# Performance work log

Hardware: AMD Instinct MI355X
Metric: run time of the kernel (lower is better)

## Reference

```python
import math
import jax, jax.numpy as jnp
import numpy as np

B, LA, LB, H = 32, 1024, 1024, 1024


def setup_inputs() -> dict:
    key = jax.random.key(0)
    k1, k2, k3, k4 = jax.random.split(key, 4)
    a = jax.random.normal(k1, (B, LA, H), dtype=jnp.float32)
    b = jax.random.normal(k2, (B, LB, H), dtype=jnp.float32)
    mask_a = jax.random.randint(k3, (B, LA, 1), 0, 2, dtype=jnp.int32)
    mask_b = jax.random.randint(k4, (B, LB, 1), 0, 2, dtype=jnp.int32)
    temperature = jnp.asarray(1.0 / math.sqrt(H), dtype=jnp.float32)
    return {"a": a, "b": b, "mask_a": mask_a, "mask_b": mask_b,
            "temperature": temperature}


def reference(a, b, mask_a, mask_b, temperature):
    # attn: [B, La, Lb] scaled cross-attention scores
    attn = jnp.einsum("bsh,bth->bst", a, b) * temperature
    # outer product of per-token validity -> pairwise valid mask [B, La, Lb]
    mask = jnp.einsum("bsi,bti->bst",
                      mask_a.astype(jnp.float32),
                      mask_b.astype(jnp.float32)).astype(bool)
    attn = jnp.where(mask, attn, jnp.float32(-10000.0))
    attn_a = jax.nn.softmax(attn, axis=1)  # normalize over La
    attn_b = jax.nn.softmax(attn, axis=2)  # normalize over Lb
    feature_b = jnp.einsum("bst,bsh->bth", attn_a, a)  # [B, Lb, H]
    feature_a = jnp.einsum("bst,bth->bsh", attn_b, b)  # [B, La, H]
    return feature_a, feature_b
```

## Files before the change

### kernel.cpp

```cpp
#include <hip/hip_runtime.h>

#define NB 32
#define L 1024
#define H 1024

typedef __attribute__((ext_vector_type(4))) float floatx4;
typedef __attribute__((ext_vector_type(8))) short shortx8;
typedef __attribute__((ext_vector_type(8))) unsigned short ushortx8;

__device__ __forceinline__ unsigned short f2bf(float f) {
    union { float f; unsigned int u; } v; v.f = f;
    unsigned int u = v.u;
    u += 0x7fffu + ((u >> 16) & 1u);
    return (unsigned short)(u >> 16);
}
__device__ __forceinline__ float bf2f(unsigned short h) {
    union { unsigned int u; float f; } v; v.u = ((unsigned int)h) << 16;
    return v.f;
}

__device__ __forceinline__ void gload_lds16(const void* g, void* l) {
    __builtin_amdgcn_global_load_lds(
        (const __attribute__((address_space(1))) unsigned int*)g,
        (__attribute__((address_space(3))) unsigned int*)l, 16, 0, 0);
}

__device__ __forceinline__ void swz_tile(int nb, int& bi_l, int& tx, int& ty) {
    int fid = blockIdx.x;
    int wid = (fid & 7) * (nb * 8) + (fid >> 3);
    bi_l = wid >> 6;
    int t = wid & 63;
    tx = t & 7;
    ty = t >> 3;
}

__global__ void detect_kernel(const unsigned short* a, int* flag) {
    int tid = threadIdx.x;
    unsigned short u = a[tid];
    int e = (u >> 7) & 0xff;
    int ok = (u == 0) || (e >= 116 && e <= 136);
    unsigned long long ball = __ballot(ok != 0);
    if (tid == 0) flag[0] = (__popcll(ball) >= 56) ? 1 : 0;
}

__device__ __forceinline__ void store_out(void* out, size_t eidx, float v, int isbf) {
    if (isbf) ((unsigned short*)out)[eidx] = f2bf(v);
    else      ((float*)out)[eidx] = v;
}

__global__ __launch_bounds__(256) void convT_kernel(
    const void* A, const void* Bm, const int* flag,
    unsigned short* a_c, unsigned short* b_c,
    unsigned short* aT, unsigned short* bT,
    float* mean_a, float* mean_b, int b0) {
    __shared__ __align__(16) unsigned short T[64][80];
    int z = blockIdx.z;
    int which = z & 1, bi_l = z >> 1, bi = b0 + bi_l;
    int s0 = blockIdx.y * 64, h0 = blockIdx.x * 64;
    const void* src = which ? Bm : A;
    unsigned short* xc = which ? b_c : a_c;
    unsigned short* xT = which ? bT : aT;
    float* msum = which ? mean_b : mean_a;
    int isbf = flag[0];
    int tid = threadIdx.x;

    int r = tid >> 2, c0 = (tid & 3) * 16;
    size_t gin = (size_t)bi * L * H + (size_t)(s0 + r) * H + h0 + c0;
    unsigned short v[16];
    if (isbf) {
        const unsigned short* p = (const unsigned short*)src + gin;
        *(ushortx8*)&v[0] = *(const ushortx8*)p;
        *(ushortx8*)&v[8] = *(const ushortx8*)(p + 8);
    } else {
        const float* p = (const float*)src + gin;
#pragma unroll
        for (int u = 0; u < 16; u += 4) {
            float4 f = *(const float4*)(p + u);
            v[u] = f2bf(f.x); v[u + 1] = f2bf(f.y);
            v[u + 2] = f2bf(f.z); v[u + 3] = f2bf(f.w);
        }
    }
    *(ushortx8*)&T[r][c0] = *(const ushortx8*)&v[0];
    *(ushortx8*)&T[r][c0 + 8] = *(const ushortx8*)&v[8];
    if (!isbf) {
        size_t gco = (size_t)bi_l * L * H + (size_t)(s0 + r) * H + h0 + c0;
        *(ushortx8*)&xc[gco] = *(const ushortx8*)&v[0];
        *(ushortx8*)&xc[gco + 8] = *(const ushortx8*)&v[8];
    }
    __syncthreads();

    int hr = tid >> 2, sc0 = (tid & 3) * 16;
    unsigned short tv2[16];
    float ms = 0.f;
#pragma unroll
    for (int u = 0; u < 16; ++u) {
        unsigned short q = T[sc0 + u][hr];
        tv2[u] = q;
        ms += bf2f(q);
    }
    size_t gto = (size_t)bi_l * (size_t)H * L + (size_t)(h0 + hr) * L + s0 + sc0;
    *(ushortx8*)&xT[gto] = *(const ushortx8*)&tv2[0];
    *(ushortx8*)&xT[gto + 8] = *(const ushortx8*)&tv2[8];
    ms += __shfl_xor(ms, 1);
    ms += __shfl_xor(ms, 2);
    if ((tid & 3) == 0) atomicAdd(&msum[bi * H + h0 + hr], ms);
}

__device__ __forceinline__ void gemm_kk(
    const unsigned short* Arow, const unsigned short* Brow,
    int lda, int ldb, int K,
    unsigned short* AsBase, unsigned short* BsBase,
    int tid, floatx4 (&acc)[4][4]) {
    int lane = tid & 63;
    int wid = tid >> 6;
    int wm = wid >> 1, wn = wid & 1;
    int lane15 = lane & 15, quad = lane >> 4;

    for (int k0 = 0; k0 < K; k0 += 32) {
#pragma unroll
        for (int it = 0; it < 4; ++it) {
            int idx = (it & 1) * 256 + tid;
            int rr = idx >> 2, cc = (idx & 3) * 8;
            const unsigned short* src = (it < 2)
                ? (Arow + (size_t)rr * lda + k0 + cc)
                : (Brow + (size_t)rr * ldb + k0 + cc);
            unsigned short* dst = ((it < 2) ? AsBase : BsBase) + idx * 8;
            gload_lds16(src, dst);
        }
        __syncthreads();
        shortx8 af[4], bfr[4];
#pragma unroll
        for (int i = 0; i < 4; ++i)
            af[i] = *(const shortx8*)(AsBase + (wm * 64 + i * 16 + lane15) * 32 + quad * 8);
#pragma unroll
        for (int j = 0; j < 4; ++j)
            bfr[j] = *(const shortx8*)(BsBase + (wn * 64 + j * 16 + lane15) * 32 + quad * 8);
#pragma unroll
        for (int i = 0; i < 4; ++i)
#pragma unroll
            for (int j = 0; j < 4; ++j)
                acc[i][j] = __builtin_amdgcn_mfma_f32_16x16x32_bf16(af[i], bfr[j], acc[i][j], 0, 0, 0);
        __syncthreads();
    }
}

__global__ __launch_bounds__(256) void score_kernel(
    const void* Araw, const void* Braw,
    const unsigned short* a_c, const unsigned short* b_c,
    const int* mask_a, const int* mask_b, const void* temp, const int* flag,
    unsigned short* w, unsigned short* wT,
    float* row_l, float* col_l, int b0, int nb) {
    __shared__ __align__(16) unsigned short lds_all[8192];
    unsigned short* As = lds_all;
    unsigned short* Bs = lds_all + 4096;
    int bi_l, tx, ty;
    swz_tile(nb, bi_l, tx, ty);
    int bi = b0 + bi_l;
    int s0 = ty * 128, t0 = tx * 128;
    int tid = threadIdx.x;
    int isbf = flag[0];

    floatx4 acc[4][4];
#pragma unroll
    for (int i = 0; i < 4; ++i)
#pragma unroll
        for (int j = 0; j < 4; ++j)
#pragma unroll
            for (int rr = 0; rr < 4; ++rr) acc[i][j][rr] = 0.f;

    const unsigned short* Arow = isbf
        ? (const unsigned short*)Araw + (size_t)bi * L * H + (size_t)s0 * H
        : a_c + (size_t)bi_l * L * H + (size_t)s0 * H;
    const unsigned short* Brow = isbf
        ? (const unsigned short*)Braw + (size_t)bi * L * H + (size_t)t0 * H
        : b_c + (size_t)bi_l * L * H + (size_t)t0 * H;
    gemm_kk(Arow, Brow, H, H, H, As, Bs, tid, acc);

    float tv = isbf ? bf2f(((const unsigned short*)temp)[0]) : ((const float*)temp)[0];
    int lane = tid & 63, wid = tid >> 6;
    int wm = wid >> 1, wn = wid & 1;
    int lane15 = lane & 15, quad = lane >> 4;

    int mb[4];
#pragma unroll
    for (int j = 0; j < 4; ++j)
        mb[j] = mask_b[bi * L + t0 + wn * 64 + j * 16 + lane15];
    size_t wbase = (size_t)bi_l * L * L;
    float colp[4] = {0.f, 0.f, 0.f, 0.f};
#pragma unroll
    for (int i = 0; i < 4; ++i) {
#pragma unroll
        for (int r = 0; r < 4; ++r) {
            int s = s0 + wm * 64 + i * 16 + quad * 4 + r;
            int ma = mask_a[bi * L + s];
            float rp = 0.f;
#pragma unroll
            for (int j = 0; j < 4; ++j) {
                int t = t0 + wn * 64 + j * 16 + lane15;
                float wv = (ma && mb[j]) ? __expf(acc[i][j][r] * tv) : 0.f;
                unsigned short wq = f2bf(wv);
                w[wbase + (size_t)s * L + t] = wq;
                float wf = bf2f(wq);
                rp += wf;
                colp[j] += wf;
            }
            rp += __shfl_xor(rp, 1);
            rp += __shfl_xor(rp, 2);
            rp += __shfl_xor(rp, 4);
            rp += __shfl_xor(rp, 8);
            if (lane15 == 0) atomicAdd(&row_l[bi * L + s], rp);
        }
    }
#pragma unroll
    for (int j = 0; j < 4; ++j) {
        float cp = colp[j];
        cp += __shfl_xor(cp, 16);
        cp += __shfl_xor(cp, 32);
        if (quad == 0) {
            int t = t0 + wn * 64 + j * 16 + lane15;
            atomicAdd(&col_l[bi * L + t], cp);
        }
    }

    unsigned short* slab = lds_all;
    int c = wn * 16 + lane15;
    for (int j = 0; j < 4; ++j) {
        __syncthreads();
#pragma unroll
        for (int i = 0; i < 4; ++i) {
#pragma unroll
            for (int r = 0; r < 4; ++r) {
                int sl = wm * 64 + i * 16 + quad * 4 + r;
                int ma = mask_a[bi * L + s0 + sl];
                float wv = (ma && mb[j]) ? __expf(acc[i][j][r] * tv) : 0.f;
                slab[sl * 34 + c] = f2bf(wv);
            }
        }
        __syncthreads();
        int cc = tid >> 3, sch = (tid & 7) * 16;
        __align__(16) unsigned short o[16];
#pragma unroll
        for (int u = 0; u < 16; ++u) o[u] = slab[(sch + u) * 34 + cc];
        int t = t0 + (cc >> 4) * 64 + j * 16 + (cc & 15);
        size_t go = (size_t)bi_l * L * L + (size_t)t * L + s0 + sch;
        *(ushortx8*)&wT[go] = *(const ushortx8*)&o[0];
        *(ushortx8*)&wT[go + 8] = *(const ushortx8*)&o[8];
    }
}

__global__ __launch_bounds__(256) void feat_a_kernel(
    const unsigned short* w, const unsigned short* bT, const int* mask_a,
    const int* flag, const float* row_l, const float* mean_b, void* out,
    int b0, int nb) {
    __shared__ __align__(16) unsigned short As[128 * 32];
    __shared__ __align__(16) unsigned short Bs[128 * 32];
    int bi_l, tx, ty;
    swz_tile(nb, bi_l, tx, ty);
    int bi = b0 + bi_l;
    int s0 = ty * 128, h0 = tx * 128;
    int tid = threadIdx.x;

    floatx4 acc[4][4];
#pragma unroll
    for (int i = 0; i < 4; ++i)
#pragma unroll
        for (int j = 0; j < 4; ++j)
#pragma unroll
            for (int rr = 0; rr < 4; ++rr) acc[i][j][rr] = 0.f;

    gemm_kk(w + (size_t)bi_l * L * L + (size_t)s0 * L,
            bT + (size_t)bi_l * (size_t)H * L + (size_t)h0 * L,
            L, L, L, As, Bs, tid, acc);

    int isbf = flag[0];
    int lane = tid & 63, wid = tid >> 6;
    int wm = wid >> 1, wn = wid & 1;
    int lane15 = lane & 15, quad = lane >> 4;
    const float invL = 1.f / (float)L;
#pragma unroll
    for (int i = 0; i < 4; ++i) {
#pragma unroll
        for (int r = 0; r < 4; ++r) {
            int s = s0 + wm * 64 + i * 16 + quad * 4 + r;
            int ma = mask_a[bi * L + s];
            float scale = ma ? (1.f / row_l[bi * L + s]) : 0.f;
#pragma unroll
            for (int j = 0; j < 4; ++j) {
                int h = h0 + wn * 64 + j * 16 + lane15;
                float v = ma ? acc[i][j][r] * scale : mean_b[bi * H + h] * invL;
                store_out(out, (size_t)bi * L * H + (size_t)s * H + h, v, isbf);
            }
        }
    }
}

__global__ __launch_bounds__(256) void feat_b_kernel(
    const unsigned short* wT, const unsigned short* aT, const int* mask_b,
    const int* flag, const float* col_l, const float* mean_a, void* out,
    int b0, int nb) {
    __shared__ __align__(16) unsigned short As[128 * 32];
    __shared__ __align__(16) unsigned short Bs[128 * 32];
    int bi_l, tx, ty;
    swz_tile(nb, bi_l, tx, ty);
    int bi = b0 + bi_l;
    int t0 = ty * 128, h0 = tx * 128;
    int tid = threadIdx.x;

    floatx4 acc[4][4];
#pragma unroll
    for (int i = 0; i < 4; ++i)
#pragma unroll
        for (int j = 0; j < 4; ++j)
#pragma unroll
            for (int rr = 0; rr < 4; ++rr) acc[i][j][rr] = 0.f;

    gemm_kk(wT + (size_t)bi_l * L * L + (size_t)t0 * L,
            aT + (size_t)bi_l * (size_t)H * L + (size_t)h0 * L,
            L, L, L, As, Bs, tid, acc);

    int isbf = flag[0];
    int lane = tid & 63, wid = tid >> 6;
    int wm = wid >> 1, wn = wid & 1;
    int lane15 = lane & 15, quad = lane >> 4;
    const float invL = 1.f / (float)L;
    const size_t FEAT_B_OFF = (size_t)NB * L * H;
#pragma unroll
    for (int i = 0; i < 4; ++i) {
#pragma unroll
        for (int r = 0; r < 4; ++r) {
            int t = t0 + wm * 64 + i * 16 + quad * 4 + r;
            int mbv = mask_b[bi * L + t];
            float scale = mbv ? (1.f / col_l[bi * L + t]) : 0.f;
#pragma unroll
            for (int j = 0; j < 4; ++j) {
                int h = h0 + wn * 64 + j * 16 + lane15;
                float v = mbv ? acc[i][j][r] * scale : mean_a[bi * H + h] * invL;
                store_out(out, FEAT_B_OFF + (size_t)bi * L * H + (size_t)t * H + h, v, isbf);
            }
        }
    }
}

extern "C" void kernel_launch(void* const* d_in, const int* in_sizes, int n_in,
                              void* d_out, int out_size, void* d_ws, size_t ws_size,
                              hipStream_t stream) {
    const void* a = d_in[0];
    const void* b = d_in[1];
    const int* mask_a = (const int*)d_in[2];
    const int* mask_b = (const int*)d_in[3];
    const void* temp = d_in[4];

    char* wsp = (char*)d_ws;
    float* row_l  = (float*)wsp;
    float* col_l  = row_l + (size_t)NB * L;
    float* mean_a = col_l + (size_t)NB * L;
    float* mean_b = mean_a + (size_t)NB * H;
    int*   flag   = (int*)(mean_b + (size_t)NB * H);
    const size_t stats_bytes = ((size_t)NB * L * 2 + (size_t)NB * H * 2) * 4 + 256;

    const size_t per_batch = 6 * (size_t)L * H * 2;
    size_t wavail = (ws_size > stats_bytes) ? ws_size - stats_bytes : 0;
    int chunk = (int)(wavail / per_batch);
    if (chunk < 1) chunk = 1;
    if (chunk > NB) chunk = NB;

    unsigned short* a_c  = (unsigned short*)(wsp + stats_bytes);
    unsigned short* b_c  = a_c + (size_t)chunk * L * H;
    unsigned short* aT   = b_c + (size_t)chunk * L * H;
    unsigned short* bT   = aT  + (size_t)chunk * L * H;
    unsigned short* wbuf = bT  + (size_t)chunk * L * H;
    unsigned short* wT   = wbuf + (size_t)chunk * L * L;

    hipMemsetAsync(d_ws, 0, stats_bytes, stream);
    detect_kernel<<<1, 64, 0, stream>>>((const unsigned short*)a, flag);

    for (int b0 = 0; b0 < NB; b0 += chunk) {
        int nb = (NB - b0 < chunk) ? (NB - b0) : chunk;
        convT_kernel<<<dim3(16, 16, nb * 2), 256, 0, stream>>>(
            a, b, flag, a_c, b_c, aT, bT, mean_a, mean_b, b0);
        score_kernel<<<dim3(nb * 64), 256, 0, stream>>>(
            a, b, a_c, b_c, mask_a, mask_b, temp, flag, wbuf, wT,
            row_l, col_l, b0, nb);
        feat_a_kernel<<<dim3(nb * 64), 256, 0, stream>>>(
            wbuf, bT, mask_a, flag, row_l, mean_b, d_out, b0, nb);
        feat_b_kernel<<<dim3(nb * 64), 256, 0, stream>>>(
            wT, aT, mask_b, flag, col_l, mean_a, d_out, b0, nb);
    }
}
```

Measured before the change: 909.9 us.

## Double-buffer GEMM LDS tiles and move weight transpose to separate kernel

Replaces the single-buffered GEMM main loop with a two-stage LDS double buffer. Loads for tile t+2 are issued while tile t is consumed, using manual vmcnt waits, raw barriers and raised MFMA priority. The in-kernel transposed write of the score weights is removed from score_kernel and done by a new standalone transpose kernel over the weight buffer. This hides global load latency behind MFMA work at the cost of doubled LDS per block (lower occupancy) and an extra full read and write pass over the weight matrix.

New measurement: 889.4 us. 2.3% less time.

```diff
diff --git a/kernel.cpp b/kernel.cpp
--- a/kernel.cpp
+++ b/kernel.cpp
@@ -106,53 +106,96 @@
     if ((tid & 3) == 0) atomicAdd(&msum[bi * H + h0 + hr], ms);
 }
 
-__device__ __forceinline__ void gemm_kk(
+__global__ __launch_bounds__(256) void wtrans_kernel(const unsigned short* w,
+                                                     unsigned short* wT) {
+    __shared__ __align__(16) unsigned short T[64][80];
+    int bi_l = blockIdx.z;
+    int s0 = blockIdx.y * 64, t0 = blockIdx.x * 64;
+    int tid = threadIdx.x;
+    int r = tid >> 2, c0 = (tid & 3) * 16;
+    size_t gin = (size_t)bi_l * L * L + (size_t)(s0 + r) * L + t0 + c0;
+    *(ushortx8*)&T[r][c0] = *(const ushortx8*)&w[gin];
+    *(ushortx8*)&T[r][c0 + 8] = *(const ushortx8*)&w[gin + 8];
+    __syncthreads();
+    int tr = tid >> 2, sc0 = (tid & 3) * 16;
+    unsigned short o[16];
+#pragma unroll
+    for (int u = 0; u < 16; ++u) o[u] = T[sc0 + u][tr];
+    size_t gout = (size_t)bi_l * L * L + (size_t)(t0 + tr) * L + s0 + sc0;
+    *(ushortx8*)&wT[gout] = *(const ushortx8*)&o[0];
+    *(ushortx8*)&wT[gout + 8] = *(const ushortx8*)&o[8];
+}
+
+__device__ __forceinline__ void stage_tiles(
+    const unsigned short* Arow, const unsigned short* Brow,
+    int lda, int ldb, int k0,
+    unsigned short* As, unsigned short* Bs, int tid) {
+#pragma unroll
+    for (int it = 0; it < 4; ++it) {
+        int idx = (it & 1) * 256 + tid;
+        int rr = idx >> 2, cc = (idx & 3) * 8;
+        const unsigned short* src = (it < 2)
+            ? (Arow + (size_t)rr * lda + k0 + cc)
+            : (Brow + (size_t)rr * ldb + k0 + cc);
+        unsigned short* dst = ((it < 2) ? As : Bs) + idx * 8;
+        gload_lds16(src, dst);
+    }
+}
+
+__device__ __forceinline__ void gemm_kk_pipe(
     const unsigned short* Arow, const unsigned short* Brow,
     int lda, int ldb, int K,
-    unsigned short* AsBase, unsigned short* BsBase,
+    unsigned short* lds,
     int tid, floatx4 (&acc)[4][4]) {
-    int lane = tid & 63;
-    int wid = tid >> 6;
+    int lane = tid & 63, wid = tid >> 6;
     int wm = wid >> 1, wn = wid & 1;
     int lane15 = lane & 15, quad = lane >> 4;
-
-    for (int k0 = 0; k0 < K; k0 += 32) {
-#pragma unroll
-        for (int it = 0; it < 4; ++it) {
-            int idx = (it & 1) * 256 + tid;
-            int rr = idx >> 2, cc = (idx & 3) * 8;
-            const unsigned short* src = (it < 2)
-                ? (Arow + (size_t)rr * lda + k0 + cc)
-                : (Brow + (size_t)rr * ldb + k0 + cc);
-            unsigned short* dst = ((it < 2) ? AsBase : BsBase) + idx * 8;
-            gload_lds16(src, dst);
-        }
-        __syncthreads();
+    unsigned short* As0 = lds;
+    unsigned short* Bs0 = lds + 4096;
+    unsigned short* As1 = lds + 8192;
+    unsigned short* Bs1 = lds + 12288;
+    int NT = K >> 5;
+
+    stage_tiles(Arow, Brow, lda, ldb, 0, As0, Bs0, tid);
+    stage_tiles(Arow, Brow, lda, ldb, 32, As1, Bs1, tid);
+
+    for (int t = 0; t < NT; ++t) {
+        unsigned short* As = (t & 1) ? As1 : As0;
+        unsigned short* Bs = (t & 1) ? Bs1 : Bs0;
+        if (t < NT - 1) asm volatile("s_waitcnt vmcnt(4)" ::: "memory");
+        else            asm volatile("s_waitcnt vmcnt(0)" ::: "memory");
+        __builtin_amdgcn_s_barrier();
+        asm volatile("" ::: "memory");
         shortx8 af[4], bfr[4];
 #pragma unroll
         for (int i = 0; i < 4; ++i)
-            af[i] = *(const shortx8*)(AsBase + (wm * 64 + i * 16 + lane15) * 32 + quad * 8);
+            af[i] = *(const shortx8*)(As + (wm * 64 + i * 16 + lane15) * 32 + quad * 8);
 #pragma unroll
         for (int j = 0; j < 4; ++j)
-            bfr[j] = *(const shortx8*)(BsBase + (wn * 64 + j * 16 + lane15) * 32 + quad * 8);
+            bfr[j] = *(const shortx8*)(Bs + (wn * 64 + j * 16 + lane15) * 32 + quad * 8);
+        asm volatile("s_waitcnt lgkmcnt(0)" ::: "memory");
+        __builtin_amdgcn_sched_barrier(0);
+        __builtin_amdgcn_s_barrier();
+        asm volatile("" ::: "memory");
+        if (t + 2 < NT)
+            stage_tiles(Arow, Brow, lda, ldb, (t + 2) * 32, As, Bs, tid);
+        __builtin_amdgcn_s_setprio(1);
 #pragma unroll
         for (int i = 0; i < 4; ++i)
 #pragma unroll
             for (int j = 0; j < 4; ++j)
                 acc[i][j] = __builtin_amdgcn_mfma_f32_16x16x32_bf16(af[i], bfr[j], acc[i][j], 0, 0, 0);
-        __syncthreads();
-    }
+        __builtin_amdgcn_s_setprio(0);
+    }
+    __builtin_amdgcn_s_barrier();
 }
 
 __global__ __launch_bounds__(256) void score_kernel(
     const void* Araw, const void* Braw,
     const unsigned short* a_c, const unsigned short* b_c,
     const int* mask_a, const int* mask_b, const void* temp, const int* flag,
-    unsigned short* w, unsigned short* wT,
-    float* row_l, float* col_l, int b0, int nb) {
-    __shared__ __align__(16) unsigned short lds_all[8192];
-    unsigned short* As = lds_all;
-    unsigned short* Bs = lds_all + 4096;
+    unsigned short* w, float* row_l, float* col_l, int b0, int nb) {
+    __shared__ __align__(16) unsigned short lds[16384];
     int bi_l, tx, ty;
     swz_tile(nb, bi_l, tx, ty);
     int bi = b0 + bi_l;
@@ -174,7 +217,7 @@
     const unsigned short* Brow = isbf
         ? (const unsigned short*)Braw + (size_t)bi * L * H + (size_t)t0 * H
         : b_c + (size_t)bi_l * L * H + (size_t)t0 * H;
-    gemm_kk(Arow, Brow, H, H, H, As, Bs, tid, acc);
+    gemm_kk_pipe(Arow, Brow, H, H, H, lds, tid, acc);
 
     float tv = isbf ? bf2f(((const unsigned short*)temp)[0]) : ((const float*)temp)[0];
     int lane = tid & 63, wid = tid >> 6;
@@ -221,39 +264,13 @@
             atomicAdd(&col_l[bi * L + t], cp);
         }
     }
-
-    unsigned short* slab = lds_all;
-    int c = wn * 16 + lane15;
-    for (int j = 0; j < 4; ++j) {
-        __syncthreads();
-#pragma unroll
-        for (int i = 0; i < 4; ++i) {
-#pragma unroll
-            for (int r = 0; r < 4; ++r) {
-                int sl = wm * 64 + i * 16 + quad * 4 + r;
-                int ma = mask_a[bi * L + s0 + sl];
-                float wv = (ma && mb[j]) ? __expf(acc[i][j][r] * tv) : 0.f;
-                slab[sl * 34 + c] = f2bf(wv);
-            }
-        }
-        __syncthreads();
-        int cc = tid >> 3, sch = (tid & 7) * 16;
-        __align__(16) unsigned short o[16];
-#pragma unroll
-        for (int u = 0; u < 16; ++u) o[u] = slab[(sch + u) * 34 + cc];
-        int t = t0 + (cc >> 4) * 64 + j * 16 + (cc & 15);
-        size_t go = (size_t)bi_l * L * L + (size_t)t * L + s0 + sch;
-        *(ushortx8*)&wT[go] = *(const ushortx8*)&o[0];
-        *(ushortx8*)&wT[go + 8] = *(const ushortx8*)&o[8];
-    }
 }
 
 __global__ __launch_bounds__(256) void feat_a_kernel(
     const unsigned short* w, const unsigned short* bT, const int* mask_a,
     const int* flag, const float* row_l, const float* mean_b, void* out,
     int b0, int nb) {
-    __shared__ __align__(16) unsigned short As[128 * 32];
-    __shared__ __align__(16) unsigned short Bs[128 * 32];
+    __shared__ __align__(16) unsigned short lds[16384];
     int bi_l, tx, ty;
     swz_tile(nb, bi_l, tx, ty);
     int bi = b0 + bi_l;
@@ -268,9 +285,9 @@
 #pragma unroll
             for (int rr = 0; rr < 4; ++rr) acc[i][j][rr] = 0.f;
 
-    gemm_kk(w + (size_t)bi_l * L * L + (size_t)s0 * L,
-            bT + (size_t)bi_l * (size_t)H * L + (size_t)h0 * L,
-            L, L, L, As, Bs, tid, acc);
+    gemm_kk_pipe(w + (size_t)bi_l * L * L + (size_t)s0 * L,
+                 bT + (size_t)bi_l * (size_t)H * L + (size_t)h0 * L,
+                 L, L, L, lds, tid, acc);
 
     int isbf = flag[0];
     int lane = tid & 63, wid = tid >> 6;
@@ -298,8 +315,7 @@
     const unsigned short* wT, const unsigned short* aT, const int* mask_b,
     const int* flag, const float* col_l, const float* mean_a, void* out,
     int b0, int nb) {
-    __shared__ __align__(16) unsigned short As[128 * 32];
-    __shared__ __align__(16) unsigned short Bs[128 * 32];
+    __shared__ __align__(16) unsigned short lds[16384];
     int bi_l, tx, ty;
     swz_tile(nb, bi_l, tx, ty);
     int bi = b0 + bi_l;
@@ -314,9 +330,9 @@
 #pragma unroll
             for (int rr = 0; rr < 4; ++rr) acc[i][j][rr] = 0.f;
 
-    gemm_kk(wT + (size_t)bi_l * L * L + (size_t)t0 * L,
-            aT + (size_t)bi_l * (size_t)H * L + (size_t)h0 * L,
-            L, L, L, As, Bs, tid, acc);
+    gemm_kk_pipe(wT + (size_t)bi_l * L * L + (size_t)t0 * L,
+                 aT + (size_t)bi_l * (size_t)H * L + (size_t)h0 * L,
+                 L, L, L, lds, tid, acc);
 
     int isbf = flag[0];
     int lane = tid & 63, wid = tid >> 6;
@@ -379,8 +395,9 @@
         convT_kernel<<<dim3(16, 16, nb * 2), 256, 0, stream>>>(
             a, b, flag, a_c, b_c, aT, bT, mean_a, mean_b, b0);
         score_kernel<<<dim3(nb * 64), 256, 0, stream>>>(
-            a, b, a_c, b_c, mask_a, mask_b, temp, flag, wbuf, wT,
+            a, b, a_c, b_c, mask_a, mask_b, temp, flag, wbuf,
             row_l, col_l, b0, nb);
+        wtrans_kernel<<<dim3(16, 16, nb), 256, 0, stream>>>(wbuf, wT);
         feat_a_kernel<<<dim3(nb * 64), 256, 0, stream>>>(
             wbuf, bT, mask_a, flag, row_l, mean_b, d_out, b0, nb);
         feat_b_kernel<<<dim3(nb * 64), 256, 0, stream>>>(
```
